# Kernel tuning notes

Measured on AMD Instinct MI355X. Metric: run time of the kernel, lower is better.

The kernel has to match this reference:

```python
import jax, jax.numpy as jnp
import numpy as np


def _reflect(i, n):
    # reflect out-of-range indices back into [0, n-1] (valid for |i| < 2n-1)
    i = jnp.abs(i)
    return jnp.where(i > n - 1, 2 * (n - 1) - i, i)


def setup_inputs() -> dict:
    key = jax.random.key(0)
    k1, k2, k3, k4, k5 = jax.random.split(key, 5)
    B, HD, T, C, H, W = 1, 2, 4, 16, 96, 96
    K = 10
    vid_in = jax.random.normal(k1, (B, HD, T, C, H, W), dtype=jnp.float32)
    dists = jax.random.uniform(k2, (B, HD, T, H, W, K), dtype=jnp.float32)
    t = jax.random.randint(k3, (B, HD, T, H, W, K), 0, T)
    r = jax.random.randint(k4, (B, HD, T, H, W, K), 0, H)
    c = jax.random.randint(k5, (B, HD, T, H, W, K), 0, W)
    inds = jnp.stack([t, r, c], axis=-1).astype(jnp.int32)
    return {"vid_in": vid_in, "dists": dists, "inds": inds,
            "ps": 7, "pt": 1, "dilation": 1}


def reference(vid_in, dists, inds, ps, pt, dilation):
    # vid_in: [B, HD, T, C, H, W]; dists: [B, HD, T, nH, nW, K];
    # inds:   [B, HD, T, nH, nW, K, 3] -> (t, row, col) top-left of patch.
    B, HD, T, C, H, W = vid_in.shape
    _, _, _, nH, nW, K = dists.shape
    vid_p = jnp.transpose(vid_in, (0, 1, 2, 4, 5, 3))  # [B,HD,T,H,W,C]

    bi = jnp.arange(B).reshape(B, 1, 1, 1, 1, 1, 1, 1)
    hi = jnp.arange(HD).reshape(1, HD, 1, 1, 1, 1, 1, 1)
    pt_off = jnp.arange(pt)
    ps_off = dilation * jnp.arange(ps)

    def body(acc, xs):
        d_k, i_k = xs  # d_k: [B,HD,T,nH,nW], i_k: [B,HD,T,nH,nW,3]
        tt = _reflect(i_k[..., 0:1] + pt_off, T)   # [B,HD,T,nH,nW,pt]
        rr = _reflect(i_k[..., 1:2] + ps_off, H)   # [B,HD,T,nH,nW,ps]
        cc = _reflect(i_k[..., 2:3] + ps_off, W)   # [B,HD,T,nH,nW,ps]
        # gathered patch values: [B,HD,T,nH,nW,pt,ps,ps,C]
        vals = vid_p[bi, hi,
                     tt[..., :, None, None],
                     rr[..., None, :, None],
                     cc[..., None, None, :]]
        acc = acc + d_k[..., None, None, None, None] * vals
        return acc, None

    acc0 = jnp.zeros((B, HD, T, nH, nW, pt, ps, ps, C), dtype=vid_in.dtype)
    xs = (jnp.moveaxis(dists, -1, 0), jnp.moveaxis(inds, -2, 0))
    acc, _ = jax.lax.scan(body, acc0, xs)
    # -> [B, HD, Q, pt, C, ps, ps]
    patches = jnp.transpose(acc, (0, 1, 2, 3, 4, 5, 8, 6, 7))
    return patches.reshape(B, HD, T * nH * nW, pt, C, ps, ps)
```

## Files before the change

kernel.cpp:

```cpp
#include <hip/hip_runtime.h>

namespace {
constexpr int HD = 2;
constexpr int T  = 4;
constexpr int C  = 16;
constexpr int H  = 96;
constexpr int W  = 96;
constexpr int K  = 10;
constexpr int PS = 7;
constexpr int HW = H * W;
constexpr int NPIX = T * HW;
constexpr int PATCH = PS * PS;
constexpr int OUTPIX = C * PATCH;
constexpr int CHUNKS = 8;
constexpr int PIX_PER_CHUNK = NPIX / CHUNKS;
constexpr int BLOCK = 1024;
constexpr int GROUPS = BLOCK / 16;
constexpr int ITERS = PIX_PER_CHUNK / GROUPS;

constexpr int WS    = 102;
constexpr int PLANE = H * WS;
constexpr int REFL  = 2 * (H - 1);
}

__global__ __launch_bounds__(BLOCK, 1)
void wpsum_kernel(const float* __restrict__ vid,
                  const float* __restrict__ dists,
                  const int* __restrict__ inds,
                  float* __restrict__ out)
{
    __shared__ float s_vid[T * PLANE];

    const int bid   = blockIdx.x;
    const int chunk = bid & (CHUNKS - 1);
    const int c     = (bid >> 3) & (C - 1);
    const int hd    = bid >> 7;

    const int tid = threadIdx.x;

    for (int t = 0; t < T; ++t) {
        const float* gsrc = vid + (size_t)((hd * T + t) * C + c) * HW;
        float*       dst  = s_vid + t * PLANE;
        for (int idx = tid; idx < H * (W / 2); idx += BLOCK) {
            const int r = idx / (W / 2);
            const int q = idx % (W / 2);
            float2 v = reinterpret_cast<const float2*>(gsrc + r * W)[q];
            reinterpret_cast<float2*>(dst + r * WS)[q] = v;
        }
        if (tid < H * (WS - W)) {
            const int r = tid / (WS - W);
            const int e = tid % (WS - W);
            dst[r * WS + W + e] = gsrc[r * W + (W - 2) - e];
        }
    }
    __syncthreads();

    const int g = tid >> 4;
    const int l = tid & 15;

    const int f0 = l, f1 = l + 16, f2 = l + 32;
    const int i0 = f0 / 7, j0 = f0 % 7;
    const int i1 = f1 / 7, j1 = f1 % 7;
    const int i2 = f2 / 7, j2 = f2 % 7;
    const int w0 = i0 * WS + j0;
    const int w1 = i1 * WS + j1;
    const int w2 = i2 * WS + j2;
    constexpr int w3 = 6 * WS + 6;
    const bool lead = (l == 0);

    const float* dbase = dists + (size_t)hd * NPIX * K;
    const int*   ibase = inds  + (size_t)hd * NPIX * K * 3;
    float*       obase = out   + (size_t)hd * NPIX * OUTPIX + (size_t)c * PATCH;

    const int pix0 = chunk * PIX_PER_CHUNK + g;

    for (int itr = 0; itr < ITERS; ++itr) {
        const int p = pix0 + itr * GROUPS;

        float2 dv[5];
        const float2* dp2 = reinterpret_cast<const float2*>(dbase + (size_t)p * K);
#pragma unroll
        for (int q = 0; q < 5; ++q) dv[q] = dp2[q];
        int2 iv[15];
        const int2* ip2 = reinterpret_cast<const int2*>(ibase + (size_t)p * (K * 3));
#pragma unroll
        for (int q = 0; q < 15; ++q) iv[q] = ip2[q];

        const float* dvf = reinterpret_cast<const float*>(dv);
        const int*   ivi = reinterpret_cast<const int*>(iv);

        float a0 = 0.f, a1 = 0.f, a2 = 0.f, a3 = 0.f;

#pragma unroll
        for (int k = 0; k < K; ++k) {
            const float d  = dvf[k];
            const int   tt = ivi[3 * k + 0];
            const int   ir = ivi[3 * k + 1];
            const int   ic = ivi[3 * k + 2];
            const int base = tt * PLANE + ic;

            if (!__any(ir > H - PS)) {
                const int b0 = base + ir * WS;
                a0 += d * s_vid[b0 + w0];
                a1 += d * s_vid[b0 + w1];
                a2 += d * s_vid[b0 + w2];
                if (lead) a3 += d * s_vid[b0 + w3];
            } else {
                const int m = REFL - ir;
                int rr;
                rr = min(ir + i0, m - i0);
                a0 += d * s_vid[base + rr * WS + j0];
                rr = min(ir + i1, m - i1);
                a1 += d * s_vid[base + rr * WS + j1];
                rr = min(ir + i2, m - i2);
                a2 += d * s_vid[base + rr * WS + j2];
                if (lead) {
                    rr = min(ir + 6, m - 6);
                    a3 += d * s_vid[base + rr * WS + 6];
                }
            }
        }

        float* op = obase + (size_t)p * OUTPIX;
        op[f0] = a0;
        op[f1] = a1;
        op[f2] = a2;
        if (lead) op[48] = a3;
    }
}

extern "C" void kernel_launch(void* const* d_in, const int* in_sizes, int n_in,
                              void* d_out, int out_size, void* d_ws, size_t ws_size,
                              hipStream_t stream) {
    const float* vid   = (const float*)d_in[0];
    const float* dists = (const float*)d_in[1];
    const int*   inds  = (const int*)d_in[2];
    float*       out   = (float*)d_out;

    dim3 grid(HD * C * CHUNKS);
    dim3 block(BLOCK);
    hipLaunchKernelGGL(wpsum_kernel, grid, block, 0, stream,
                       vid, dists, inds, out);
}
```

Before: 359.3 us.

## Store video in shared memory as half2 channel pairs and accumulate with hfma2

Each block now handles two channels, packing them as __half2 in shared memory and accumulating with packed half FMAs. This halves the index/dist global reloads per channel and the LDS instructions per output. Chunks double so the grid size stays the same. Accumulating in fp16 reduces numerical precision and may exceed the tolerance against the fp32 reference.

```diff
diff --git a/kernel.cpp b/kernel.cpp
--- a/kernel.cpp
+++ b/kernel.cpp
@@ -1,4 +1,5 @@
 #include <hip/hip_runtime.h>
+#include <hip/hip_fp16.h>
 
 namespace {
 constexpr int HD = 2;
@@ -12,13 +13,13 @@
 constexpr int NPIX = T * HW;
 constexpr int PATCH = PS * PS;
 constexpr int OUTPIX = C * PATCH;
-constexpr int CHUNKS = 8;
+constexpr int CHUNKS = 16;
 constexpr int PIX_PER_CHUNK = NPIX / CHUNKS;
 constexpr int BLOCK = 1024;
 constexpr int GROUPS = BLOCK / 16;
 constexpr int ITERS = PIX_PER_CHUNK / GROUPS;
 
-constexpr int WS    = 102;
+constexpr int WS    = 104;
 constexpr int PLANE = H * WS;
 constexpr int REFL  = 2 * (H - 1);
 }
@@ -29,28 +30,32 @@
                   const int* __restrict__ inds,
                   float* __restrict__ out)
 {
-    __shared__ float s_vid[T * PLANE];
+    __shared__ __half2 s_vid[T * PLANE];
 
     const int bid   = blockIdx.x;
     const int chunk = bid & (CHUNKS - 1);
-    const int c     = (bid >> 3) & (C - 1);
+    const int cp    = (bid >> 4) & 7;
     const int hd    = bid >> 7;
-
-    const int tid = threadIdx.x;
+    const int c0    = cp * 2;
+    const int tid   = threadIdx.x;
 
     for (int t = 0; t < T; ++t) {
-        const float* gsrc = vid + (size_t)((hd * T + t) * C + c) * HW;
-        float*       dst  = s_vid + t * PLANE;
+        const float* g0 = vid + (size_t)((hd * T + t) * C + c0) * HW;
+        const float* g1 = g0 + HW;
+        __half2* dst = s_vid + t * PLANE;
         for (int idx = tid; idx < H * (W / 2); idx += BLOCK) {
             const int r = idx / (W / 2);
             const int q = idx % (W / 2);
-            float2 v = reinterpret_cast<const float2*>(gsrc + r * W)[q];
-            reinterpret_cast<float2*>(dst + r * WS)[q] = v;
+            float2 v0 = reinterpret_cast<const float2*>(g0 + r * W)[q];
+            float2 v1 = reinterpret_cast<const float2*>(g1 + r * W)[q];
+            dst[r * WS + 2 * q]     = __floats2half2_rn(v0.x, v1.x);
+            dst[r * WS + 2 * q + 1] = __floats2half2_rn(v0.y, v1.y);
         }
-        if (tid < H * (WS - W)) {
-            const int r = tid / (WS - W);
-            const int e = tid % (WS - W);
-            dst[r * WS + W + e] = gsrc[r * W + (W - 2) - e];
+        if (tid < H * 6) {
+            const int r = tid / 6;
+            const int e = tid % 6;
+            const int sc = r * W + (W - 2) - e;
+            dst[r * WS + W + e] = __floats2half2_rn(g0[sc], g1[sc]);
         }
     }
     __syncthreads();
@@ -70,7 +75,7 @@
 
     const float* dbase = dists + (size_t)hd * NPIX * K;
     const int*   ibase = inds  + (size_t)hd * NPIX * K * 3;
-    float*       obase = out   + (size_t)hd * NPIX * OUTPIX + (size_t)c * PATCH;
+    float*       obase = out   + (size_t)hd * NPIX * OUTPIX + (size_t)c0 * PATCH;
 
     const int pix0 = chunk * PIX_PER_CHUNK + g;
 
@@ -89,43 +94,53 @@
         const float* dvf = reinterpret_cast<const float*>(dv);
         const int*   ivi = reinterpret_cast<const int*>(iv);
 
-        float a0 = 0.f, a1 = 0.f, a2 = 0.f, a3 = 0.f;
+        __half2 dh[K];
+#pragma unroll
+        for (int k = 0; k < K; ++k) dh[k] = __float2half2_rn(dvf[k]);
+
+        __half2 a0 = __float2half2_rn(0.f);
+        __half2 a1 = a0, a2 = a0, a3 = a0;
 
 #pragma unroll
         for (int k = 0; k < K; ++k) {
-            const float d  = dvf[k];
-            const int   tt = ivi[3 * k + 0];
-            const int   ir = ivi[3 * k + 1];
-            const int   ic = ivi[3 * k + 2];
+            const int tt = ivi[3 * k + 0];
+            const int ir = ivi[3 * k + 1];
+            const int ic = ivi[3 * k + 2];
             const int base = tt * PLANE + ic;
 
             if (!__any(ir > H - PS)) {
                 const int b0 = base + ir * WS;
-                a0 += d * s_vid[b0 + w0];
-                a1 += d * s_vid[b0 + w1];
-                a2 += d * s_vid[b0 + w2];
-                if (lead) a3 += d * s_vid[b0 + w3];
+                a0 = __hfma2(dh[k], s_vid[b0 + w0], a0);
+                a1 = __hfma2(dh[k], s_vid[b0 + w1], a1);
+                a2 = __hfma2(dh[k], s_vid[b0 + w2], a2);
+                if (lead) a3 = __hfma2(dh[k], s_vid[b0 + w3], a3);
             } else {
                 const int m = REFL - ir;
                 int rr;
                 rr = min(ir + i0, m - i0);
-                a0 += d * s_vid[base + rr * WS + j0];
+                a0 = __hfma2(dh[k], s_vid[base + rr * WS + j0], a0);
                 rr = min(ir + i1, m - i1);
-                a1 += d * s_vid[base + rr * WS + j1];
+                a1 = __hfma2(dh[k], s_vid[base + rr * WS + j1], a1);
                 rr = min(ir + i2, m - i2);
-                a2 += d * s_vid[base + rr * WS + j2];
+                a2 = __hfma2(dh[k], s_vid[base + rr * WS + j2], a2);
                 if (lead) {
                     rr = min(ir + 6, m - 6);
-                    a3 += d * s_vid[base + rr * WS + 6];
+                    a3 = __hfma2(dh[k], s_vid[base + rr * WS + 6], a3);
                 }
             }
         }
 
         float* op = obase + (size_t)p * OUTPIX;
-        op[f0] = a0;
-        op[f1] = a1;
-        op[f2] = a2;
-        if (lead) op[48] = a3;
+        const float2 r0 = __half22float2(a0);
+        const float2 r1 = __half22float2(a1);
+        const float2 r2 = __half22float2(a2);
+        op[f0] = r0.x;  op[f0 + PATCH] = r0.y;
+        op[f1] = r1.x;  op[f1 + PATCH] = r1.y;
+        op[f2] = r2.x;  op[f2 + PATCH] = r2.y;
+        if (lead) {
+            const float2 r3 = __half22float2(a3);
+            op[48] = r3.x;  op[48 + PATCH] = r3.y;
+        }
     }
 }
 
@@ -137,7 +152,7 @@
     const int*   inds  = (const int*)d_in[2];
     float*       out   = (float*)d_out;
 
-    dim3 grid(HD * C * CHUNKS);
+    dim3 grid(HD * (C / 2) * CHUNKS);
     dim3 block(BLOCK);
     hipLaunchKernelGGL(wpsum_kernel, grid, block, 0, stream,
                        vid, dists, inds, out);
```

Result: faster. 329.5 us (-8.3%).
